# Kernel tuning notes

Hardware: AMD Instinct MI355X
Metric: run time of the kernel (lower is better)

The kernel has to match this reference:

```python
import jax, jax.numpy as jnp
import numpy as np

N = 15000000
BSZ = 4096
D = 2048
GAMMA = 0.8
TAU_INIT = 0.5
TAU_MIN = 0.05
TAU_MAX = 1.0
RHO = 0.8
ETA_INIT = 0.001
BETA_U = 0.9
GRAD_CLIP = 3.0


def setup_inputs() -> dict:
    key = jax.random.key(0)
    k1, k2 = jax.random.split(key)
    features = jax.random.normal(k1, (2 * BSZ, D), dtype=jnp.float32)
    index = jax.random.randint(k2, (BSZ,), 0, N)
    s = jnp.zeros((N,), jnp.float32)
    tau_buf = jnp.ones((N,), jnp.float32) * TAU_INIT
    u_buf = jnp.zeros((N,), jnp.float32)
    return {"features": features, "s": s, "tau_buf": tau_buf,
            "u_buf": u_buf, "index": index, "epoch": 1}


def reference(features, s, tau_buf, u_buf, index, epoch):
    B = features.shape[0] // 2
    num_neg = 2 * B - 2
    # F.normalize(features, dim=1)
    nrm = jnp.linalg.norm(features, axis=1, keepdims=True)
    f = features / jnp.maximum(nrm, 1e-12)
    sim = f @ f.T  # [2B, 2B]
    pos_sim = jnp.concatenate([jnp.diagonal(sim, offset=B),
                               jnp.diagonal(sim, offset=-B)])[:, None]  # [2B,1]
    tau = jnp.tile(tau_buf[index], 2)  # [2B]
    # sim_d_temps is detached in the torch code
    sim_d = jax.lax.stop_gradient(sim / tau[:, None])
    mask_neg = jnp.tile(1.0 - jnp.eye(B, dtype=sim.dtype), (2, 2))  # [2B,2B]
    exp_sd = jnp.exp(sim_d) * mask_neg
    g = jnp.sum(exp_sd, axis=1) / num_neg  # [2B]
    if epoch == 0:
        s1, s2 = g[:B], g[B:]
    else:
        s_old = s[index]
        s1 = (1.0 - GAMMA) * s_old + GAMMA * g[:B]
        s2 = (1.0 - GAMMA) * s_old + GAMMA * g[B:]
    s_new = s.at[index].set((s1 + s2) / 2.0)
    # s1/s2 derive from detached quantities + non-grad buffer in torch
    s1g = jax.lax.stop_gradient(s1)
    s2g = jax.lax.stop_gradient(s2)
    w1 = exp_sd[:B] / s1g[:, None]
    w2 = exp_sd[B:] / s2g[:, None]
    loss_1 = jnp.sum(w1 * sim[:B], axis=1, keepdims=True) / num_neg - pos_sim[:B]
    loss_2 = jnp.sum(w2 * sim[B:], axis=1, keepdims=True) / num_neg - pos_sim[B:]
    loss = (loss_1 + loss_2).mean()
    # temperature (tau) gradient estimate and buffer updates
    gt1 = jnp.log(s1g) + RHO - jnp.sum(w1 * sim_d[:B], axis=1) / num_neg
    gt2 = jnp.log(s2g) + RHO - jnp.sum(w2 * sim_d[B:], axis=1) / num_neg
    grad_tau = jnp.clip((gt1 + gt2) / 2.0, -GRAD_CLIP, GRAD_CLIP)
    u_new = (1.0 - BETA_U) * u_buf[index] + BETA_U * grad_tau
    tau_new = jnp.clip(tau_buf[index] - ETA_INIT * u_new, TAU_MIN, TAU_MAX)
    u_buf_new = u_buf.at[index].set(u_new)
    tau_buf_new = tau_buf.at[index].set(tau_new)
    return loss, s_new, u_buf_new, tau_buf_new
```

## Files before the change

### kernel.cpp

```cpp
#include <hip/hip_runtime.h>
#include <hip/hip_bf16.h>
#include <stdint.h>

#define B_SZ   4096
#define TWO_B  8192
#define D_DIM  2048
#define N_TOT  15000000
#define RHO    0.8f
#define NT     32
#define NJOB   1024
#define NSLV   256
#define GT     512
#define INV_SC (1.0f/256.0f)

typedef __attribute__((ext_vector_type(4))) float f32x4;

__device__ __forceinline__ float waveReduceSum(float v) {
#pragma unroll
    for (int off = 32; off >= 1; off >>= 1) v += __shfl_down(v, off, 64);
    return v;
}
__device__ __forceinline__ void gload_lds16(const void* g, void* l) {
    __builtin_amdgcn_global_load_lds(
        (const __attribute__((address_space(1))) void*)(uintptr_t)g,
        (__attribute__((address_space(3))) void*)(uintptr_t)l,
        16, 0, 0);
}
__device__ __forceinline__ unsigned pk4(float a, float b, float c, float d) {
    int r = 0;
    r = __builtin_amdgcn_cvt_pk_fp8_f32(a, b, r, false);
    r = __builtin_amdgcn_cvt_pk_fp8_f32(c, d, r, true);
    return (unsigned)r;
}

__global__ __launch_bounds__(256) void knorm2(const float* __restrict__ feat,
                                              unsigned char* __restrict__ f8,
                                              float* __restrict__ posdot) {
    int i = blockIdx.x;
    int tid = threadIdx.x;
    const float4* ra = reinterpret_cast<const float4*>(feat + (size_t)i * D_DIM);
    const float4* rb = reinterpret_cast<const float4*>(feat + (size_t)(i + B_SZ) * D_DIM);
    float4 a0 = ra[tid * 2], a1 = ra[tid * 2 + 1];
    float4 b0 = rb[tid * 2], b1 = rb[tid * 2 + 1];
    float sa = a0.x*a0.x + a0.y*a0.y + a0.z*a0.z + a0.w*a0.w
             + a1.x*a1.x + a1.y*a1.y + a1.z*a1.z + a1.w*a1.w;
    float sb = b0.x*b0.x + b0.y*b0.y + b0.z*b0.z + b0.w*b0.w
             + b1.x*b1.x + b1.y*b1.y + b1.z*b1.z + b1.w*b1.w;
    float dp = a0.x*b0.x + a0.y*b0.y + a0.z*b0.z + a0.w*b0.w
             + a1.x*b1.x + a1.y*b1.y + a1.z*b1.z + a1.w*b1.w;
    sa = waveReduceSum(sa);
    sb = waveReduceSum(sb);
    dp = waveReduceSum(dp);
    __shared__ float wsum[3][4];
    if ((tid & 63) == 0) {
        int wv = tid >> 6;
        wsum[0][wv] = sa; wsum[1][wv] = sb; wsum[2][wv] = dp;
    }
    __syncthreads();
    float ta = wsum[0][0] + wsum[0][1] + wsum[0][2] + wsum[0][3];
    float tb = wsum[1][0] + wsum[1][1] + wsum[1][2] + wsum[1][3];
    float td = wsum[2][0] + wsum[2][1] + wsum[2][2] + wsum[2][3];
    float ia = 1.0f / fmaxf(sqrtf(ta), 1e-12f);
    float ib = 1.0f / fmaxf(sqrtf(tb), 1e-12f);
    if (tid == 0) posdot[i] = td * ia * ib;
    float xa = ia * 16.0f, xb = ib * 16.0f;
    uint2 oa, ob;
    oa.x = pk4(a0.x * xa, a0.y * xa, a0.z * xa, a0.w * xa);
    oa.y = pk4(a1.x * xa, a1.y * xa, a1.z * xa, a1.w * xa);
    ob.x = pk4(b0.x * xb, b0.y * xb, b0.z * xb, b0.w * xb);
    ob.y = pk4(b1.x * xb, b1.y * xb, b1.z * xb, b1.w * xb);
    reinterpret_cast<uint2*>(f8 + (size_t)i * D_DIM)[tid] = oa;
    reinterpret_cast<uint2*>(f8 + (size_t)(i + B_SZ) * D_DIM)[tid] = ob;
}

__global__ __launch_bounds__(GT, 4) void kgram(
        const unsigned char* __restrict__ f8,
        const float* __restrict__ tau_buf, const int* __restrict__ index,
        float* __restrict__ E, float* __restrict__ F,
        const float4* __restrict__ sIn, const float4* __restrict__ uIn,
        const float4* __restrict__ tIn, float* __restrict__ out) {
    const int raw = (int)blockIdx.x;
    const int bid = (raw & 7) * (NJOB / 8) + (raw >> 3);
    int C = (int)((sqrtf((float)(4 * bid + 1)) - 1.0f) * 0.5f);
    while (C * C + C > bid) --C;
    while ((C + 1) * (C + 1) + (C + 1) <= bid) ++C;
    const int R = bid - C * C - C;
    const int r0 = R * 128, c0 = C * 256;

    const int tid = threadIdx.x;
    const int lane = tid & 63;
    const int w = tid >> 6;
    const int wr = w >> 2;
    const int wc = w & 3;
    const int l15 = lane & 15, lhi = lane >> 4;

    __shared__ alignas(16) unsigned char As[3][128 * 64];
    __shared__ alignas(16) unsigned char Bs[3][256 * 64];

    f32x4 acc[4][4] = {};

    const int rr = lane >> 2;
    const int sj = (lane & 3) ^ ((rr >> 1) & 3);
    const size_t gA  = (size_t)(r0 + w * 16 + rr) * D_DIM + sj * 16;
    const size_t gB0 = (size_t)(c0 + w * 32 + rr) * D_DIM + sj * 16;
    const size_t gB1 = gB0 + 16 * D_DIM;
    const int lA = w * 1024, lB0 = w * 2048, lB1 = w * 2048 + 1024;

#define STAGE(buf, t)                                              \
    do {                                                           \
        size_t k_ = (size_t)(t) * 64u;                             \
        gload_lds16(f8 + gA + k_,  &As[buf][lA]);                  \
        gload_lds16(f8 + gB0 + k_, &Bs[buf][lB0]);                 \
        gload_lds16(f8 + gB1 + k_, &Bs[buf][lB1]);                 \
    } while (0)

    STAGE(0, 0);
    STAGE(1, 1);
    asm volatile("s_waitcnt vmcnt(3)" ::: "memory");
    __builtin_amdgcn_sched_barrier(0);
    __builtin_amdgcn_s_barrier();

    const int kx = (l15 >> 1) & 3;
    const int pk0 = (((lhi >> 1) ^ kx) * 16) + (lhi & 1) * 8;
    const int pk1 = ((((lhi >> 1) + 2) ^ kx) * 16) + (lhi & 1) * 8;

    int bufc = 0;
    for (int t = 0; t < NT; ++t) {
        if (t + 2 < NT) {
            int bw = (bufc >= 1) ? bufc - 1 : 2;
            STAGE(bw, t + 2);
        }
        const unsigned char* __restrict__ A_l = &As[bufc][0];
        const unsigned char* __restrict__ B_l = &Bs[bufc][0];
        long af[4][2], bfr[4][2];
#pragma unroll
        for (int m = 0; m < 4; ++m) {
            int rowb = (wr * 64 + m * 16 + l15) * 64;
            af[m][0] = *reinterpret_cast<const long*>(&A_l[rowb + pk0]);
            af[m][1] = *reinterpret_cast<const long*>(&A_l[rowb + pk1]);
        }
#pragma unroll
        for (int n = 0; n < 4; ++n) {
            int rowb = (wc * 64 + n * 16 + l15) * 64;
            bfr[n][0] = *reinterpret_cast<const long*>(&B_l[rowb + pk0]);
            bfr[n][1] = *reinterpret_cast<const long*>(&B_l[rowb + pk1]);
        }
        __builtin_amdgcn_s_setprio(1);
#pragma unroll
        for (int m = 0; m < 4; ++m)
#pragma unroll
            for (int n = 0; n < 4; ++n) {
                acc[m][n] = __builtin_amdgcn_mfma_f32_16x16x32_fp8_fp8(af[m][0], bfr[n][0], acc[m][n], 0, 0, 0);
                acc[m][n] = __builtin_amdgcn_mfma_f32_16x16x32_fp8_fp8(af[m][1], bfr[n][1], acc[m][n], 0, 0, 0);
            }
        __builtin_amdgcn_s_setprio(0);
        if (t < NT - 2) {
            asm volatile("s_waitcnt vmcnt(3)" ::: "memory");
        } else if (t == NT - 2) {
            asm volatile("s_waitcnt vmcnt(0)" ::: "memory");
        }
        __builtin_amdgcn_sched_barrier(0);
        if (t < NT - 1) __builtin_amdgcn_s_barrier();
        bufc = (bufc == 2) ? 0 : bufc + 1;
    }
#undef STAGE

#pragma unroll
    for (int m = 0; m < 4; ++m) {
#pragma unroll
        for (int r = 0; r < 4; ++r) {
            int row_g = r0 + wr * 64 + m * 16 + lhi * 4 + r;
            float it = 1.0f / tau_buf[index[row_g & (B_SZ - 1)]];
            float e = 0.f, f = 0.f;
#pragma unroll
            for (int n = 0; n < 4; ++n) {
                int col_g = c0 + wc * 64 + n * 16 + l15;
                float v = acc[m][n][r] * INV_SC;
                if (col_g > row_g && (((row_g ^ col_g) & (B_SZ - 1)) != 0)) {
                    float ex = __expf(v * it);
                    e += ex;
                    f += ex * v;
                }
            }
#pragma unroll
            for (int off = 1; off < 16; off <<= 1) {
                e += __shfl_xor(e, off, 64);
                f += __shfl_xor(f, off, 64);
            }
            if (l15 == 0) {
                atomicAdd(&E[row_g], e);
                atomicAdd(&F[row_g], f);
            }
        }
    }
#pragma unroll
    for (int n = 0; n < 4; ++n) {
        int colT = c0 + wc * 64 + n * 16 + l15;
        float it = 1.0f / tau_buf[index[colT & (B_SZ - 1)]];
        float e = 0.f, f = 0.f;
#pragma unroll
        for (int m = 0; m < 4; ++m) {
#pragma unroll
            for (int r = 0; r < 4; ++r) {
                int row_g = r0 + wr * 64 + m * 16 + lhi * 4 + r;
                float v = acc[m][n][r] * INV_SC;
                if (colT > row_g && (((row_g ^ colT) & (B_SZ - 1)) != 0)) {
                    float ex = __expf(v * it);
                    e += ex;
                    f += ex * v;
                }
            }
        }
        e += __shfl_xor(e, 16, 64);
        f += __shfl_xor(f, 16, 64);
        e += __shfl_xor(e, 32, 64);
        f += __shfl_xor(f, 32, 64);
        if (lhi == 0) {
            atomicAdd(&E[colT], e);
            atomicAdd(&F[colT], f);
        }
    }

    {
        typedef float4 __attribute__((aligned(4))) float4u;
        size_t i = (size_t)raw * GT + tid;
        const size_t stride = (size_t)NJOB * GT;
        const size_t n4 = N_TOT / 4;
        for (; i < n4; i += stride) {
            *reinterpret_cast<float4u*>(out + 1 + 4 * i) = sIn[i];
            *reinterpret_cast<float4u*>(out + 1 + (size_t)N_TOT + 4 * i) = uIn[i];
            *reinterpret_cast<float4u*>(out + 1 + 2 * (size_t)N_TOT + 4 * i) = tIn[i];
        }
    }
}

__global__ __launch_bounds__(GT, 4) void ksliver(
        const unsigned char* __restrict__ f8,
        const float* __restrict__ tau_buf, const int* __restrict__ index,
        float* __restrict__ E, float* __restrict__ F) {
    const int sb = (int)blockIdx.x;
    const int R = 32 + (sb >> 3);
    const int sv = sb & 7;
    const int r0 = R * 128 + sv * 16;
    const int c0 = 31 * 256;

    const int tid = threadIdx.x;
    const int lane = tid & 63;
    const int w = tid >> 6;
    const int l15 = lane & 15, lhi = lane >> 4;

    __shared__ alignas(16) unsigned char As[3][16 * 64];
    __shared__ alignas(16) unsigned char Bs[3][256 * 64];

    f32x4 acc[2] = {};

    const int rr = lane >> 2;
    const int sj = (lane & 3) ^ ((rr >> 1) & 3);
    const size_t gA  = (size_t)(r0 + rr) * D_DIM + sj * 16;
    const size_t gB0 = (size_t)(c0 + w * 32 + rr) * D_DIM + sj * 16;
    const size_t gB1 = gB0 + 16 * D_DIM;
    const int lB0 = w * 2048, lB1 = w * 2048 + 1024;

#define STAGE(buf, t)                                              \
    do {                                                           \
        size_t k_ = (size_t)(t) * 64u;                             \
        gload_lds16(f8 + gA + k_,  &As[buf][0]);                   \
        gload_lds16(f8 + gB0 + k_, &Bs[buf][lB0]);                 \
        gload_lds16(f8 + gB1 + k_, &Bs[buf][lB1]);                 \
    } while (0)

    STAGE(0, 0);
    STAGE(1, 1);
    asm volatile("s_waitcnt vmcnt(3)" ::: "memory");
    __builtin_amdgcn_sched_barrier(0);
    __builtin_amdgcn_s_barrier();

    const int kx = (l15 >> 1) & 3;
    const int pk0 = (((lhi >> 1) ^ kx) * 16) + (lhi & 1) * 8;
    const int pk1 = ((((lhi >> 1) + 2) ^ kx) * 16) + (lhi & 1) * 8;

    int bufc = 0;
    for (int t = 0; t < NT; ++t) {
        if (t + 2 < NT) {
            int bw = (bufc >= 1) ? bufc - 1 : 2;
            STAGE(bw, t + 2);
        }
        const unsigned char* __restrict__ A_l = &As[bufc][0];
        const unsigned char* __restrict__ B_l = &Bs[bufc][0];
        long af0, af1, bfr[2][2];
        {
            int rowb = l15 * 64;
            af0 = *reinterpret_cast<const long*>(&A_l[rowb + pk0]);
            af1 = *reinterpret_cast<const long*>(&A_l[rowb + pk1]);
        }
#pragma unroll
        for (int n = 0; n < 2; ++n) {
            int rowb = (w * 32 + n * 16 + l15) * 64;
            bfr[n][0] = *reinterpret_cast<const long*>(&B_l[rowb + pk0]);
            bfr[n][1] = *reinterpret_cast<const long*>(&B_l[rowb + pk1]);
        }
        __builtin_amdgcn_s_setprio(1);
#pragma unroll
        for (int n = 0; n < 2; ++n) {
            acc[n] = __builtin_amdgcn_mfma_f32_16x16x32_fp8_fp8(af0, bfr[n][0], acc[n], 0, 0, 0);
            acc[n] = __builtin_amdgcn_mfma_f32_16x16x32_fp8_fp8(af1, bfr[n][1], acc[n], 0, 0, 0);
        }
        __builtin_amdgcn_s_setprio(0);
        if (t < NT - 2) {
            asm volatile("s_waitcnt vmcnt(3)" ::: "memory");
        } else if (t == NT - 2) {
            asm volatile("s_waitcnt vmcnt(0)" ::: "memory");
        }
        __builtin_amdgcn_sched_barrier(0);
        if (t < NT - 1) __builtin_amdgcn_s_barrier();
        bufc = (bufc == 2) ? 0 : bufc + 1;
    }
#undef STAGE

#pragma unroll
    for (int r = 0; r < 4; ++r) {
        int row_g = r0 + lhi * 4 + r;
        float it = 1.0f / tau_buf[index[row_g & (B_SZ - 1)]];
        float e = 0.f, f = 0.f;
#pragma unroll
        for (int n = 0; n < 2; ++n) {
            int col_g = c0 + w * 32 + n * 16 + l15;
            float v = acc[n][r] * INV_SC;
            if (col_g > row_g && (((row_g ^ col_g) & (B_SZ - 1)) != 0)) {
                float ex = __expf(v * it);
                e += ex;
                f += ex * v;
            }
        }
#pragma unroll
        for (int off = 1; off < 16; off <<= 1) {
            e += __shfl_xor(e, off, 64);
            f += __shfl_xor(f, off, 64);
        }
        if (l15 == 0) {
            atomicAdd(&E[row_g], e);
            atomicAdd(&F[row_g], f);
        }
    }
#pragma unroll
    for (int n = 0; n < 2; ++n) {
        int colT = c0 + w * 32 + n * 16 + l15;
        float it = 1.0f / tau_buf[index[colT & (B_SZ - 1)]];
        float e = 0.f, f = 0.f;
#pragma unroll
        for (int r = 0; r < 4; ++r) {
            int row_g = r0 + lhi * 4 + r;
            float v = acc[n][r] * INV_SC;
            if (colT > row_g && (((row_g ^ colT) & (B_SZ - 1)) != 0)) {
                float ex = __expf(v * it);
                e += ex;
                f += ex * v;
            }
        }
        e += __shfl_xor(e, 16, 64);
        f += __shfl_xor(f, 16, 64);
        e += __shfl_xor(e, 32, 64);
        f += __shfl_xor(f, 32, 64);
        if (lhi == 0) {
            atomicAdd(&E[colT], e);
            atomicAdd(&F[colT], f);
        }
    }
}

__global__ __launch_bounds__(64) void kfin(const float* __restrict__ E,
                                           const float* __restrict__ F,
                                           const float* __restrict__ posdot,
                                           const float* __restrict__ s,
                                           const float* __restrict__ tau_buf,
                                           const float* __restrict__ u_buf,
                                           const int* __restrict__ index,
                                           const int* __restrict__ epoch_p,
                                           float* __restrict__ out) {
    int i = blockIdx.x;
    int lane = threadIdx.x;
    int idx = index[i];
    bool dup = false;
    for (int j = i + 1 + lane; j < B_SZ; j += 64)
        if (index[j] == idx) dup = true;
    unsigned long long ball = __ballot(dup);

    if (lane == 0) {
        float e1 = E[i], f1 = F[i];
        float e2 = E[i + B_SZ], f2 = F[i + B_SZ];
        const float num_neg = 2.0f * B_SZ - 2.0f;
        float g1 = e1 / num_neg, g2 = e2 / num_neg;
        float s_old = s[idx];
        float tau_i = tau_buf[idx];
        float u_old = u_buf[idx];
        int ep = *epoch_p;
        float s1, s2;
        if (ep == 0) { s1 = g1; s2 = g2; }
        else { s1 = 0.2f * s_old + 0.8f * g1; s2 = 0.2f * s_old + 0.8f * g2; }
        float pos = posdot[i];
        float l1 = f1 / (s1 * num_neg) - pos;
        float l2 = f2 / (s2 * num_neg) - pos;
        atomicAdd(out, (l1 + l2) * (1.0f / B_SZ));
        float gt1 = logf(s1) + RHO - f1 / (tau_i * s1 * num_neg);
        float gt2 = logf(s2) + RHO - f2 / (tau_i * s2 * num_neg);
        float gt = 0.5f * (gt1 + gt2);
        gt = fminf(fmaxf(gt, -3.0f), 3.0f);
        float u_new = 0.1f * u_old + 0.9f * gt;
        float tau_new = fminf(fmaxf(tau_i - 0.001f * u_new, 0.05f), 1.0f);
        if (ball == 0ULL) {
            out[1 + (size_t)idx] = 0.5f * (s1 + s2);
            out[1 + (size_t)N_TOT + idx] = u_new;
            out[1 + 2 * (size_t)N_TOT + idx] = tau_new;
        }
    }
}

extern "C" void kernel_launch(void* const* d_in, const int* in_sizes, int n_in,
                              void* d_out, int out_size, void* d_ws, size_t ws_size,
                              hipStream_t stream) {
    const float* features = (const float*)d_in[0];
    const float* s        = (const float*)d_in[1];
    const float* tau_buf  = (const float*)d_in[2];
    const float* u_buf    = (const float*)d_in[3];
    const int*   index    = (const int*)d_in[4];
    const int*   epoch    = (const int*)d_in[5];
    float* out = (float*)d_out;
    char* ws = (char*)d_ws;

    unsigned char* f8     = (unsigned char*)(ws);
    float*         E      = (float*)(ws + 16777216);
    float*         F      = (float*)(ws + 16809984);
    float*         posdot = (float*)(ws + 16842752);

    hipMemsetAsync(d_out, 0, sizeof(float), stream);
    hipMemsetAsync(E, 0, 2 * TWO_B * sizeof(float), stream);

    knorm2<<<B_SZ, 256, 0, stream>>>(features, f8, posdot);
    kgram<<<NJOB, GT, 0, stream>>>(f8, tau_buf, index, E, F,
                                   (const float4*)s, (const float4*)u_buf,
                                   (const float4*)tau_buf, out);
    ksliver<<<NSLV, GT, 0, stream>>>(f8, tau_buf, index, E, F);
    kfin<<<B_SZ, 64, 0, stream>>>(E, F, posdot, s, tau_buf, u_buf, index, epoch, out);
}
```

Measured before the change: 299.4 us.

## Merge gram and sliver kernels, add dedicated copy wave, fold memsets into norm kernel

Merges the gram tile kernel and the sliver kernel into one launch of 1280 blocks. Each block gets a ninth wave that streams the large s/u/tau buffer copy in step with the MFMA loop, matching its s_barrier count. The two memsets are folded into the normalization kernel, which removes launches and overlaps the memory-bound copy with compute. In exchange, 576-thread blocks may lower occupancy, and the barrier matching between the copy wave and compute waves is fragile, especially for sliver blocks.

```diff
diff --git a/kernel.cpp b/kernel.cpp
--- a/kernel.cpp
+++ b/kernel.cpp
@@ -10,10 +10,11 @@
 #define NT     32
 #define NJOB   1024
 #define NSLV   256
-#define GT     512
+#define NBLK   1280
 #define INV_SC (1.0f/256.0f)
 
 typedef __attribute__((ext_vector_type(4))) float f32x4;
+typedef float4 __attribute__((aligned(4))) float4u;
 
 __device__ __forceinline__ float waveReduceSum(float v) {
 #pragma unroll
@@ -35,9 +36,17 @@
 
 __global__ __launch_bounds__(256) void knorm2(const float* __restrict__ feat,
                                               unsigned char* __restrict__ f8,
-                                              float* __restrict__ posdot) {
+                                              float* __restrict__ posdot,
+                                              float* __restrict__ EF,
+                                              float* __restrict__ out) {
     int i = blockIdx.x;
     int tid = threadIdx.x;
+    if (i < 16) {
+        float4 z = make_float4(0.f, 0.f, 0.f, 0.f);
+        reinterpret_cast<float4*>(EF)[i * 256 + tid] = z;
+    }
+    if (i == 16 && tid == 0) out[0] = 0.f;
+
     const float4* ra = reinterpret_cast<const float4*>(feat + (size_t)i * D_DIM);
     const float4* rb = reinterpret_cast<const float4*>(feat + (size_t)(i + B_SZ) * D_DIM);
     float4 a0 = ra[tid * 2], a1 = ra[tid * 2 + 1];
@@ -73,40 +82,65 @@
     reinterpret_cast<uint2*>(f8 + (size_t)(i + B_SZ) * D_DIM)[tid] = ob;
 }
 
-__global__ __launch_bounds__(GT, 4) void kgram(
+__global__ __launch_bounds__(576) void kbig(
         const unsigned char* __restrict__ f8,
         const float* __restrict__ tau_buf, const int* __restrict__ index,
         float* __restrict__ E, float* __restrict__ F,
         const float4* __restrict__ sIn, const float4* __restrict__ uIn,
         const float4* __restrict__ tIn, float* __restrict__ out) {
     const int raw = (int)blockIdx.x;
-    const int bid = (raw & 7) * (NJOB / 8) + (raw >> 3);
-    int C = (int)((sqrtf((float)(4 * bid + 1)) - 1.0f) * 0.5f);
-    while (C * C + C > bid) --C;
-    while ((C + 1) * (C + 1) + (C + 1) <= bid) ++C;
-    const int R = bid - C * C - C;
-    const int r0 = R * 128, c0 = C * 256;
-
     const int tid = threadIdx.x;
     const int lane = tid & 63;
     const int w = tid >> 6;
-    const int wr = w >> 2;
-    const int wc = w & 3;
     const int l15 = lane & 15, lhi = lane >> 4;
 
     __shared__ alignas(16) unsigned char As[3][128 * 64];
     __shared__ alignas(16) unsigned char Bs[3][256 * 64];
 
-    f32x4 acc[4][4] = {};
-
+    if (w == 8) {
+        size_t g = (size_t)raw * 64 + lane;
+        const size_t n4 = N_TOT / 4;
+        const size_t str = (size_t)NBLK * 64;
+        __builtin_amdgcn_s_barrier();
+        for (int t = 0; t < NT; ++t) {
+#pragma unroll
+            for (int k = 0; k < 2; ++k) {
+                size_t i = g + (size_t)(2 * t + k) * str;
+                if (i < n4) {
+                    float4 vs = sIn[i], vu = uIn[i], vt = tIn[i];
+                    *reinterpret_cast<float4u*>(out + 1 + 4 * i) = vs;
+                    *reinterpret_cast<float4u*>(out + 1 + (size_t)N_TOT + 4 * i) = vu;
+                    *reinterpret_cast<float4u*>(out + 1 + 2 * (size_t)N_TOT + 4 * i) = vt;
+                }
+            }
+            if (t < NT - 1) __builtin_amdgcn_s_barrier();
+        }
+        return;
+    }
+
+    const int kx = (l15 >> 1) & 3;
+    const int pk0 = (((lhi >> 1) ^ kx) * 16) + (lhi & 1) * 8;
+    const int pk1 = ((((lhi >> 1) + 2) ^ kx) * 16) + (lhi & 1) * 8;
     const int rr = lane >> 2;
     const int sj = (lane & 3) ^ ((rr >> 1) & 3);
-    const size_t gA  = (size_t)(r0 + w * 16 + rr) * D_DIM + sj * 16;
-    const size_t gB0 = (size_t)(c0 + w * 32 + rr) * D_DIM + sj * 16;
-    const size_t gB1 = gB0 + 16 * D_DIM;
-    const int lA = w * 1024, lB0 = w * 2048, lB1 = w * 2048 + 1024;
-
-#define STAGE(buf, t)                                              \
+
+    if (raw < NJOB) {
+        const int bid = (raw & 7) * (NJOB / 8) + (raw >> 3);
+        int C = (int)((sqrtf((float)(4 * bid + 1)) - 1.0f) * 0.5f);
+        while (C * C + C > bid) --C;
+        while ((C + 1) * (C + 1) + (C + 1) <= bid) ++C;
+        const int R = bid - C * C - C;
+        const int r0 = R * 128, c0 = C * 256;
+        const int wr = w >> 2, wc = w & 3;
+
+        f32x4 acc[4][4] = {};
+
+        const size_t gA  = (size_t)(r0 + w * 16 + rr) * D_DIM + sj * 16;
+        const size_t gB0 = (size_t)(c0 + w * 32 + rr) * D_DIM + sj * 16;
+        const size_t gB1 = gB0 + 16 * D_DIM;
+        const int lA = w * 1024, lB0 = w * 2048, lB1 = w * 2048 + 1024;
+
+#define STAGEM(buf, t)                                             \
     do {                                                           \
         size_t k_ = (size_t)(t) * 64u;                             \
         gload_lds16(f8 + gA + k_,  &As[buf][lA]);                  \
@@ -114,154 +148,123 @@
         gload_lds16(f8 + gB1 + k_, &Bs[buf][lB1]);                 \
     } while (0)
 
-    STAGE(0, 0);
-    STAGE(1, 1);
-    asm volatile("s_waitcnt vmcnt(3)" ::: "memory");
-    __builtin_amdgcn_sched_barrier(0);
-    __builtin_amdgcn_s_barrier();
-
-    const int kx = (l15 >> 1) & 3;
-    const int pk0 = (((lhi >> 1) ^ kx) * 16) + (lhi & 1) * 8;
-    const int pk1 = ((((lhi >> 1) + 2) ^ kx) * 16) + (lhi & 1) * 8;
-
-    int bufc = 0;
-    for (int t = 0; t < NT; ++t) {
-        if (t + 2 < NT) {
-            int bw = (bufc >= 1) ? bufc - 1 : 2;
-            STAGE(bw, t + 2);
-        }
-        const unsigned char* __restrict__ A_l = &As[bufc][0];
-        const unsigned char* __restrict__ B_l = &Bs[bufc][0];
-        long af[4][2], bfr[4][2];
-#pragma unroll
-        for (int m = 0; m < 4; ++m) {
-            int rowb = (wr * 64 + m * 16 + l15) * 64;
-            af[m][0] = *reinterpret_cast<const long*>(&A_l[rowb + pk0]);
-            af[m][1] = *reinterpret_cast<const long*>(&A_l[rowb + pk1]);
-        }
-#pragma unroll
-        for (int n = 0; n < 4; ++n) {
-            int rowb = (wc * 64 + n * 16 + l15) * 64;
-            bfr[n][0] = *reinterpret_cast<const long*>(&B_l[rowb + pk0]);
-            bfr[n][1] = *reinterpret_cast<const long*>(&B_l[rowb + pk1]);
-        }
-        __builtin_amdgcn_s_setprio(1);
-#pragma unroll
-        for (int m = 0; m < 4; ++m)
+        STAGEM(0, 0);
+        STAGEM(1, 1);
+        asm volatile("s_waitcnt vmcnt(3)" ::: "memory");
+        __builtin_amdgcn_sched_barrier(0);
+        __builtin_amdgcn_s_barrier();
+
+        int bufc = 0;
+        for (int t = 0; t < NT; ++t) {
+            if (t + 2 < NT) {
+                int bw = (bufc >= 1) ? bufc - 1 : 2;
+                STAGEM(bw, t + 2);
+            }
+            const unsigned char* __restrict__ A_l = &As[bufc][0];
+            const unsigned char* __restrict__ B_l = &Bs[bufc][0];
+            long af[4][2], bfr[4][2];
+#pragma unroll
+            for (int m = 0; m < 4; ++m) {
+                int rowb = (wr * 64 + m * 16 + l15) * 64;
+                af[m][0] = *reinterpret_cast<const long*>(&A_l[rowb + pk0]);
+                af[m][1] = *reinterpret_cast<const long*>(&A_l[rowb + pk1]);
+            }
 #pragma unroll
             for (int n = 0; n < 4; ++n) {
-                acc[m][n] = __builtin_amdgcn_mfma_f32_16x16x32_fp8_fp8(af[m][0], bfr[n][0], acc[m][n], 0, 0, 0);
-                acc[m][n] = __builtin_amdgcn_mfma_f32_16x16x32_fp8_fp8(af[m][1], bfr[n][1], acc[m][n], 0, 0, 0);
-            }
-        __builtin_amdgcn_s_setprio(0);
-        if (t < NT - 2) {
-            asm volatile("s_waitcnt vmcnt(3)" ::: "memory");
-        } else if (t == NT - 2) {
-            asm volatile("s_waitcnt vmcnt(0)" ::: "memory");
-        }
-        __builtin_amdgcn_sched_barrier(0);
-        if (t < NT - 1) __builtin_amdgcn_s_barrier();
-        bufc = (bufc == 2) ? 0 : bufc + 1;
-    }
-#undef STAGE
-
-#pragma unroll
-    for (int m = 0; m < 4; ++m) {
-#pragma unroll
-        for (int r = 0; r < 4; ++r) {
-            int row_g = r0 + wr * 64 + m * 16 + lhi * 4 + r;
-            float it = 1.0f / tau_buf[index[row_g & (B_SZ - 1)]];
-            float e = 0.f, f = 0.f;
-#pragma unroll
-            for (int n = 0; n < 4; ++n) {
-                int col_g = c0 + wc * 64 + n * 16 + l15;
-                float v = acc[m][n][r] * INV_SC;
-                if (col_g > row_g && (((row_g ^ col_g) & (B_SZ - 1)) != 0)) {
-                    float ex = __expf(v * it);
-                    e += ex;
-                    f += ex * v;
-                }
-            }
-#pragma unroll
-            for (int off = 1; off < 16; off <<= 1) {
-                e += __shfl_xor(e, off, 64);
-                f += __shfl_xor(f, off, 64);
-            }
-            if (l15 == 0) {
-                atomicAdd(&E[row_g], e);
-                atomicAdd(&F[row_g], f);
-            }
-        }
-    }
-#pragma unroll
-    for (int n = 0; n < 4; ++n) {
-        int colT = c0 + wc * 64 + n * 16 + l15;
-        float it = 1.0f / tau_buf[index[colT & (B_SZ - 1)]];
-        float e = 0.f, f = 0.f;
+                int rowb = (wc * 64 + n * 16 + l15) * 64;
+                bfr[n][0] = *reinterpret_cast<const long*>(&B_l[rowb + pk0]);
+                bfr[n][1] = *reinterpret_cast<const long*>(&B_l[rowb + pk1]);
+            }
+            __builtin_amdgcn_s_setprio(1);
+#pragma unroll
+            for (int m = 0; m < 4; ++m)
+#pragma unroll
+                for (int n = 0; n < 4; ++n) {
+                    acc[m][n] = __builtin_amdgcn_mfma_f32_16x16x32_fp8_fp8(af[m][0], bfr[n][0], acc[m][n], 0, 0, 0);
+                    acc[m][n] = __builtin_amdgcn_mfma_f32_16x16x32_fp8_fp8(af[m][1], bfr[n][1], acc[m][n], 0, 0, 0);
+                }
+            __builtin_amdgcn_s_setprio(0);
+            if (t < NT - 2) {
+                asm volatile("s_waitcnt vmcnt(3)" ::: "memory");
+            } else if (t == NT - 2) {
+                asm volatile("s_waitcnt vmcnt(0)" ::: "memory");
+            }
+            __builtin_amdgcn_sched_barrier(0);
+            if (t < NT - 1) __builtin_amdgcn_s_barrier();
+            bufc = (bufc == 2) ? 0 : bufc + 1;
+        }
+#undef STAGEM
+
 #pragma unroll
         for (int m = 0; m < 4; ++m) {
 #pragma unroll
             for (int r = 0; r < 4; ++r) {
                 int row_g = r0 + wr * 64 + m * 16 + lhi * 4 + r;
-                float v = acc[m][n][r] * INV_SC;
-                if (colT > row_g && (((row_g ^ colT) & (B_SZ - 1)) != 0)) {
-                    float ex = __expf(v * it);
-                    e += ex;
-                    f += ex * v;
-                }
-            }
-        }
-        e += __shfl_xor(e, 16, 64);
-        f += __shfl_xor(f, 16, 64);
-        e += __shfl_xor(e, 32, 64);
-        f += __shfl_xor(f, 32, 64);
-        if (lhi == 0) {
-            atomicAdd(&E[colT], e);
-            atomicAdd(&F[colT], f);
-        }
-    }
-
-    {
-        typedef float4 __attribute__((aligned(4))) float4u;
-        size_t i = (size_t)raw * GT + tid;
-        const size_t stride = (size_t)NJOB * GT;
-        const size_t n4 = N_TOT / 4;
-        for (; i < n4; i += stride) {
-            *reinterpret_cast<float4u*>(out + 1 + 4 * i) = sIn[i];
-            *reinterpret_cast<float4u*>(out + 1 + (size_t)N_TOT + 4 * i) = uIn[i];
-            *reinterpret_cast<float4u*>(out + 1 + 2 * (size_t)N_TOT + 4 * i) = tIn[i];
-        }
-    }
-}
-
-__global__ __launch_bounds__(GT, 4) void ksliver(
-        const unsigned char* __restrict__ f8,
-        const float* __restrict__ tau_buf, const int* __restrict__ index,
-        float* __restrict__ E, float* __restrict__ F) {
-    const int sb = (int)blockIdx.x;
-    const int R = 32 + (sb >> 3);
-    const int sv = sb & 7;
-    const int r0 = R * 128 + sv * 16;
-    const int c0 = 31 * 256;
-
-    const int tid = threadIdx.x;
-    const int lane = tid & 63;
-    const int w = tid >> 6;
-    const int l15 = lane & 15, lhi = lane >> 4;
-
-    __shared__ alignas(16) unsigned char As[3][16 * 64];
-    __shared__ alignas(16) unsigned char Bs[3][256 * 64];
-
-    f32x4 acc[2] = {};
-
-    const int rr = lane >> 2;
-    const int sj = (lane & 3) ^ ((rr >> 1) & 3);
-    const size_t gA  = (size_t)(r0 + rr) * D_DIM + sj * 16;
-    const size_t gB0 = (size_t)(c0 + w * 32 + rr) * D_DIM + sj * 16;
-    const size_t gB1 = gB0 + 16 * D_DIM;
-    const int lB0 = w * 2048, lB1 = w * 2048 + 1024;
-
-#define STAGE(buf, t)                                              \
+                float it = 1.0f / tau_buf[index[row_g & (B_SZ - 1)]];
+                float e = 0.f, f = 0.f;
+#pragma unroll
+                for (int n = 0; n < 4; ++n) {
+                    int col_g = c0 + wc * 64 + n * 16 + l15;
+                    float v = acc[m][n][r] * INV_SC;
+                    if (col_g > row_g && (((row_g ^ col_g) & (B_SZ - 1)) != 0)) {
+                        float ex = __expf(v * it);
+                        e += ex;
+                        f += ex * v;
+                    }
+                }
+#pragma unroll
+                for (int off = 1; off < 16; off <<= 1) {
+                    e += __shfl_xor(e, off, 64);
+                    f += __shfl_xor(f, off, 64);
+                }
+                if (l15 == 0) {
+                    atomicAdd(&E[row_g], e);
+                    atomicAdd(&F[row_g], f);
+                }
+            }
+        }
+#pragma unroll
+        for (int n = 0; n < 4; ++n) {
+            int colT = c0 + wc * 64 + n * 16 + l15;
+            float it = 1.0f / tau_buf[index[colT & (B_SZ - 1)]];
+            float e = 0.f, f = 0.f;
+#pragma unroll
+            for (int m = 0; m < 4; ++m) {
+#pragma unroll
+                for (int r = 0; r < 4; ++r) {
+                    int row_g = r0 + wr * 64 + m * 16 + lhi * 4 + r;
+                    float v = acc[m][n][r] * INV_SC;
+                    if (colT > row_g && (((row_g ^ colT) & (B_SZ - 1)) != 0)) {
+                        float ex = __expf(v * it);
+                        e += ex;
+                        f += ex * v;
+                    }
+                }
+            }
+            e += __shfl_xor(e, 16, 64);
+            f += __shfl_xor(f, 16, 64);
+            e += __shfl_xor(e, 32, 64);
+            f += __shfl_xor(f, 32, 64);
+            if (lhi == 0) {
+                atomicAdd(&E[colT], e);
+                atomicAdd(&F[colT], f);
+            }
+        }
+    } else {
+        const int sb = raw - NJOB;
+        const int R = 32 + (sb >> 3);
+        const int sv = sb & 7;
+        const int r0 = R * 128 + sv * 16;
+        const int c0 = 31 * 256;
+
+        f32x4 acc[2] = {};
+
+        const size_t gA  = (size_t)(r0 + rr) * D_DIM + sj * 16;
+        const size_t gB0 = (size_t)(c0 + w * 32 + rr) * D_DIM + sj * 16;
+        const size_t gB1 = gB0 + 16 * D_DIM;
+        const int lB0 = w * 2048, lB1 = w * 2048 + 1024;
+
+#define STAGES(buf, t)                                             \
     do {                                                           \
         size_t k_ = (size_t)(t) * 64u;                             \
         gload_lds16(f8 + gA + k_,  &As[buf][0]);                   \
@@ -269,101 +272,98 @@
         gload_lds16(f8 + gB1 + k_, &Bs[buf][lB1]);                 \
     } while (0)
 
-    STAGE(0, 0);
-    STAGE(1, 1);
-    asm volatile("s_waitcnt vmcnt(3)" ::: "memory");
-    __builtin_amdgcn_sched_barrier(0);
-    __builtin_amdgcn_s_barrier();
-
-    const int kx = (l15 >> 1) & 3;
-    const int pk0 = (((lhi >> 1) ^ kx) * 16) + (lhi & 1) * 8;
-    const int pk1 = ((((lhi >> 1) + 2) ^ kx) * 16) + (lhi & 1) * 8;
-
-    int bufc = 0;
-    for (int t = 0; t < NT; ++t) {
-        if (t + 2 < NT) {
-            int bw = (bufc >= 1) ? bufc - 1 : 2;
-            STAGE(bw, t + 2);
-        }
-        const unsigned char* __restrict__ A_l = &As[bufc][0];
-        const unsigned char* __restrict__ B_l = &Bs[bufc][0];
-        long af0, af1, bfr[2][2];
-        {
-            int rowb = l15 * 64;
-            af0 = *reinterpret_cast<const long*>(&A_l[rowb + pk0]);
-            af1 = *reinterpret_cast<const long*>(&A_l[rowb + pk1]);
-        }
-#pragma unroll
-        for (int n = 0; n < 2; ++n) {
-            int rowb = (w * 32 + n * 16 + l15) * 64;
-            bfr[n][0] = *reinterpret_cast<const long*>(&B_l[rowb + pk0]);
-            bfr[n][1] = *reinterpret_cast<const long*>(&B_l[rowb + pk1]);
-        }
-        __builtin_amdgcn_s_setprio(1);
-#pragma unroll
-        for (int n = 0; n < 2; ++n) {
-            acc[n] = __builtin_amdgcn_mfma_f32_16x16x32_fp8_fp8(af0, bfr[n][0], acc[n], 0, 0, 0);
-            acc[n] = __builtin_amdgcn_mfma_f32_16x16x32_fp8_fp8(af1, bfr[n][1], acc[n], 0, 0, 0);
-        }
-        __builtin_amdgcn_s_setprio(0);
-        if (t < NT - 2) {
-            asm volatile("s_waitcnt vmcnt(3)" ::: "memory");
-        } else if (t == NT - 2) {
-            asm volatile("s_waitcnt vmcnt(0)" ::: "memory");
-        }
+        STAGES(0, 0);
+        STAGES(1, 1);
+        asm volatile("s_waitcnt vmcnt(3)" ::: "memory");
         __builtin_amdgcn_sched_barrier(0);
-        if (t < NT - 1) __builtin_amdgcn_s_barrier();
-        bufc = (bufc == 2) ? 0 : bufc + 1;
-    }
-#undef STAGE
-
-#pragma unroll
-    for (int r = 0; r < 4; ++r) {
-        int row_g = r0 + lhi * 4 + r;
-        float it = 1.0f / tau_buf[index[row_g & (B_SZ - 1)]];
-        float e = 0.f, f = 0.f;
-#pragma unroll
-        for (int n = 0; n < 2; ++n) {
-            int col_g = c0 + w * 32 + n * 16 + l15;
-            float v = acc[n][r] * INV_SC;
-            if (col_g > row_g && (((row_g ^ col_g) & (B_SZ - 1)) != 0)) {
-                float ex = __expf(v * it);
-                e += ex;
-                f += ex * v;
-            }
-        }
-#pragma unroll
-        for (int off = 1; off < 16; off <<= 1) {
-            e += __shfl_xor(e, off, 64);
-            f += __shfl_xor(f, off, 64);
-        }
-        if (l15 == 0) {
-            atomicAdd(&E[row_g], e);
-            atomicAdd(&F[row_g], f);
-        }
-    }
-#pragma unroll
-    for (int n = 0; n < 2; ++n) {
-        int colT = c0 + w * 32 + n * 16 + l15;
-        float it = 1.0f / tau_buf[index[colT & (B_SZ - 1)]];
-        float e = 0.f, f = 0.f;
+        __builtin_amdgcn_s_barrier();
+
+        int bufc = 0;
+        for (int t = 0; t < NT; ++t) {
+            if (t + 2 < NT) {
+                int bw = (bufc >= 1) ? bufc - 1 : 2;
+                STAGES(bw, t + 2);
+            }
+            const unsigned char* __restrict__ A_l = &As[bufc][0];
+            const unsigned char* __restrict__ B_l = &Bs[bufc][0];
+            long af0, af1, bfr[2][2];
+            {
+                int rowb = l15 * 64;
+                af0 = *reinterpret_cast<const long*>(&A_l[rowb + pk0]);
+                af1 = *reinterpret_cast<const long*>(&A_l[rowb + pk1]);
+            }
+#pragma unroll
+            for (int n = 0; n < 2; ++n) {
+                int rowb = (w * 32 + n * 16 + l15) * 64;
+                bfr[n][0] = *reinterpret_cast<const long*>(&B_l[rowb + pk0]);
+                bfr[n][1] = *reinterpret_cast<const long*>(&B_l[rowb + pk1]);
+            }
+            __builtin_amdgcn_s_setprio(1);
+#pragma unroll
+            for (int n = 0; n < 2; ++n) {
+                acc[n] = __builtin_amdgcn_mfma_f32_16x16x32_fp8_fp8(af0, bfr[n][0], acc[n], 0, 0, 0);
+                acc[n] = __builtin_amdgcn_mfma_f32_16x16x32_fp8_fp8(af1, bfr[n][1], acc[n], 0, 0, 0);
+            }
+            __builtin_amdgcn_s_setprio(0);
+            if (t < NT - 2) {
+                asm volatile("s_waitcnt vmcnt(3)" ::: "memory");
+            } else if (t == NT - 2) {
+                asm volatile("s_waitcnt vmcnt(0)" ::: "memory");
+            }
+            __builtin_amdgcn_sched_barrier(0);
+            if (t < NT - 1) __builtin_amdgcn_s_barrier();
+            bufc = (bufc == 2) ? 0 : bufc + 1;
+        }
+#undef STAGES
+
 #pragma unroll
         for (int r = 0; r < 4; ++r) {
             int row_g = r0 + lhi * 4 + r;
-            float v = acc[n][r] * INV_SC;
-            if (colT > row_g && (((row_g ^ colT) & (B_SZ - 1)) != 0)) {
-                float ex = __expf(v * it);
-                e += ex;
-                f += ex * v;
-            }
-        }
-        e += __shfl_xor(e, 16, 64);
-        f += __shfl_xor(f, 16, 64);
-        e += __shfl_xor(e, 32, 64);
-        f += __shfl_xor(f, 32, 64);
-        if (lhi == 0) {
-            atomicAdd(&E[colT], e);
-            atomicAdd(&F[colT], f);
+            float it = 1.0f / tau_buf[index[row_g & (B_SZ - 1)]];
+            float e = 0.f, f = 0.f;
+#pragma unroll
+            for (int n = 0; n < 2; ++n) {
+                int col_g = c0 + w * 32 + n * 16 + l15;
+                float v = acc[n][r] * INV_SC;
+                if (col_g > row_g && (((row_g ^ col_g) & (B_SZ - 1)) != 0)) {
+                    float ex = __expf(v * it);
+                    e += ex;
+                    f += ex * v;
+                }
+            }
+#pragma unroll
+            for (int off = 1; off < 16; off <<= 1) {
+                e += __shfl_xor(e, off, 64);
+                f += __shfl_xor(f, off, 64);
+            }
+            if (l15 == 0) {
+                atomicAdd(&E[row_g], e);
+                atomicAdd(&F[row_g], f);
+            }
+        }
+#pragma unroll
+        for (int n = 0; n < 2; ++n) {
+            int colT = c0 + w * 32 + n * 16 + l15;
+            float it = 1.0f / tau_buf[index[colT & (B_SZ - 1)]];
+            float e = 0.f, f = 0.f;
+#pragma unroll
+            for (int r = 0; r < 4; ++r) {
+                int row_g = r0 + lhi * 4 + r;
+                float v = acc[n][r] * INV_SC;
+                if (colT > row_g && (((row_g ^ colT) & (B_SZ - 1)) != 0)) {
+                    float ex = __expf(v * it);
+                    e += ex;
+                    f += ex * v;
+                }
+            }
+            e += __shfl_xor(e, 16, 64);
+            f += __shfl_xor(f, 16, 64);
+            e += __shfl_xor(e, 32, 64);
+            f += __shfl_xor(f, 32, 64);
+            if (lhi == 0) {
+                atomicAdd(&E[colT], e);
+                atomicAdd(&F[colT], f);
+            }
         }
     }
 }
@@ -432,13 +432,9 @@
     float*         F      = (float*)(ws + 16809984);
     float*         posdot = (float*)(ws + 16842752);
 
-    hipMemsetAsync(d_out, 0, sizeof(float), stream);
-    hipMemsetAsync(E, 0, 2 * TWO_B * sizeof(float), stream);
-
-    knorm2<<<B_SZ, 256, 0, stream>>>(features, f8, posdot);
-    kgram<<<NJOB, GT, 0, stream>>>(f8, tau_buf, index, E, F,
+    knorm2<<<B_SZ, 256, 0, stream>>>(features, f8, posdot, E, out);
+    kbig<<<NBLK, 576, 0, stream>>>(f8, tau_buf, index, E, F,
                                    (const float4*)s, (const float4*)u_buf,
                                    (const float4*)tau_buf, out);
-    ksliver<<<NSLV, GT, 0, stream>>>(f8, tau_buf, index, E, F);
     kfin<<<B_SZ, 64, 0, stream>>>(E, F, posdot, s, tau_buf, u_buf, index, epoch, out);
 }
```

Measured after the change: 375.2 us. 1.25x slower.
